# Optimization experiments

Measured on AMD Instinct MI355X. Metric: run time of the kernel, lower is better.

Reference implementation:

```python
import jax, jax.numpy as jnp
import numpy as np

FILTER_LENGTHS = (2, 4)  # from module: self.filter_length = [2, 4]


def _get_conv(signal, b, h, l, d_k, conv, w):
    # signal: [b, h*d_k, l] (raw reshape of [b,h,l,d_k], matching torch .reshape)
    f = max(FILTER_LENGTHS)
    pad = f // 2
    padded = jnp.pad(signal, ((0, 0), (0, 0), (pad, pad)))  # [b, d, l+f]
    # unfold(-1, f, 1)[:, :, :l, :] -> sliding windows, keep first l
    idx = jnp.arange(l)[:, None] + jnp.arange(f)[None, :]  # [l, f]
    seq = padded[:, :, idx]  # [b, d, l, f]
    # dynamic filter-length selection: w_f = filter_lengths * w, pick argmax
    f_s = jnp.asarray(FILTER_LENGTHS, dtype=signal.dtype)
    ind = jnp.argmax(f_s * w)
    chosen_len = jnp.asarray(FILTER_LENGTHS)[ind]
    mask = (jnp.arange(f) < chosen_len).astype(signal.dtype)  # [f]
    seq = seq * mask  # broadcast over [b, d, l, f]
    # depthwise-ish conv via einsum, then raw reshape (b, l, h*d_k) -> (b, h, l, d_k)
    out = jnp.einsum('bdlf,dof->blo', seq, conv)
    return out.reshape(b, h, l, d_k)


def reference(Q, K, V, attn_mask, conv_q, conv_k, w):
    b, h, l, d_k = Q.shape
    Qc = _get_conv(Q.reshape(b, h * d_k, l), b, h, l, d_k, conv_q, w) + Q
    Kc = _get_conv(K.reshape(b, h * d_k, l), b, h, l, d_k, conv_k, w) + K
    scores = jnp.einsum('bhqd,bhkd->bhqk', Qc, Kc) / np.sqrt(d_k).astype(Q.dtype)
    attn = jax.nn.softmax(scores, axis=-1)
    context = jnp.einsum('bhqk,bhkd->bhqd', attn, V)
    return context, attn


def setup_inputs() -> dict:
    key = jax.random.key(0)
    ks = jax.random.split(key, 6)
    b, h, l, d_k = 4, 8, 2048, 64
    d = h * d_k
    f = max(FILTER_LENGTHS)
    return {
        'Q': jax.random.normal(ks[0], (b, h, l, d_k), dtype=jnp.float32),
        'K': jax.random.normal(ks[1], (b, h, l, d_k), dtype=jnp.float32),
        'V': jax.random.normal(ks[2], (b, h, l, d_k), dtype=jnp.float32),
        'attn_mask': jnp.zeros((b, 1, l, l), dtype=bool),  # unused by forward
        'conv_q': jax.random.normal(ks[3], (d, d, f), dtype=jnp.float32),
        'conv_k': jax.random.normal(ks[4], (d, d, f), dtype=jnp.float32),
        'w': jax.random.normal(ks[5], (2,), dtype=jnp.float32),
    }
```

## Files before the change

### kernel.cpp

```cpp
#include <hip/hip_runtime.h>

typedef _Float16 f16;
typedef _Float16 f16x4 __attribute__((ext_vector_type(4)));
typedef _Float16 f16x8 __attribute__((ext_vector_type(8)));
typedef float f32x4 __attribute__((ext_vector_type(4)));
typedef float f32x16 __attribute__((ext_vector_type(16)));

#define MFMA32(A, B, C) __builtin_amdgcn_mfma_f32_32x32x16_f16(A, B, C, 0, 0, 0)

constexpr int Bb = 4, Hh = 8, Ll = 2048, Dk = 64, Dm = 512, BH = 32;

constexpr size_t NWF = (size_t)16 * 128 * 64 * 8;
constexpr size_t NFF = (size_t)BH * 64 * 4 * 64 * 8;
constexpr size_t NVF = (size_t)BH * 2 * 128 * 64 * 8;

constexpr size_t OFF_WF = 256;
constexpr size_t OFF_FF = OFF_WF + 4 * NWF * sizeof(f16);
constexpr size_t OFF_VF = OFF_FF + 4 * NFF * sizeof(f16);

#define QSCALE 0.1803368801111204f

__global__ void kprep_w(const float* __restrict__ convq, const float* __restrict__ convk,
                        const float* __restrict__ w, int* __restrict__ flag,
                        f16* __restrict__ wfhq, f16* __restrict__ wflq,
                        f16* __restrict__ wfhk, f16* __restrict__ wflk) {
    const int len = (4.f * w[1] > 2.f * w[0]) ? 4 : 2;
    if (blockIdx.x == 0 && blockIdx.y == 0 && threadIdx.x == 0) *flag = len;
    int g = blockIdx.x * 256 + threadIdx.x;
    int o = g & 511, c8 = g >> 9;
    const float* conv = blockIdx.y ? convk : convq;
    f16* dh = blockIdx.y ? wfhk : wfhq;
    f16* dl = blockIdx.y ? wflk : wflq;
    float4 v[8];
#pragma unroll
    for (int cc = 0; cc < 8; ++cc)
        v[cc] = *(const float4*)(conv + ((size_t)(c8 * 8 + cc) * 512 + o) * 4);
    int ob = o >> 5;
#pragma unroll
    for (int f = 0; f < 4; ++f) {
        f16x8 hv, lv;
#pragma unroll
        for (int cc = 0; cc < 8; ++cc) {
            float x = (f < len) ? ((const float*)&v[cc])[f] : 0.f;
            f16 hi = (f16)x;
            hv[cc] = hi; lv[cc] = (f16)(x - (float)hi);
        }
        int k16 = f * 32 + (c8 >> 1);
        size_t base = (((size_t)ob * 128 + k16) * 64 + (c8 & 1) * 32 + (o & 31)) * 8;
        *(f16x8*)(dh + base) = hv;
        *(f16x8*)(dl + base) = lv;
    }
}

__global__ void kprep_v(const float* __restrict__ V, f16* __restrict__ vf) {
    int bh = blockIdx.y, l0 = blockIdx.x * 128;
    int tid = threadIdx.x;
    const float* src = V + (size_t)bh * Ll * Dk;
#pragma unroll
    for (int s = 0; s < 4; ++s) {
        int g = s * 4 + (tid >> 6);
        int lane = tid & 63;
        int l16s = g >> 1, db = g & 1;
        int khalf = lane >> 5, lane31 = lane & 31;
        int d = db * 32 + lane31;
        f16x8 out;
#pragma unroll
        for (int j = 0; j < 8; ++j) {
            int l = l0 + l16s * 16 + khalf * 8 + j;
            out[j] = (f16)src[(size_t)l * Dk + d];
        }
        size_t idx = ((((size_t)bh * 2 + db) * 128 + (l0 >> 4) + l16s) * 64 + lane) * 8;
        *(f16x8*)(vf + idx) = out;
    }
}

__global__ __launch_bounds__(256, 4) void kconv(
    const float* __restrict__ Q, const float* __restrict__ K, const int* __restrict__ flag,
    const f16* __restrict__ wfhq, const f16* __restrict__ wflq,
    const f16* __restrict__ wfhk, const f16* __restrict__ wflk,
    f16* __restrict__ ffhq, f16* __restrict__ fflq,
    f16* __restrict__ ffhk, f16* __restrict__ fflk) {
    __shared__ __align__(16) f16 est[4][2][32][40];
    int id = blockIdx.x;
    int xcd = id & 7, oTile = (id >> 3) & 3, gidx = id >> 5;
    int g = gidx * 8 + xcd;
    int tt = g & 31, b = (g >> 5) & 3, tensor = (g >> 7) & 1;
    int wave = threadIdx.x >> 6, lane = threadIdx.x & 63;
    int wn = wave & 1, wm = wave >> 1;
    int lane31 = lane & 31, khalf = lane >> 5;
    const f16* bhp = (tensor ? wfhk : wfhq) + ((size_t)(oTile * 4 + wn * 2) * 128) * 512;
    const f16* blp = (tensor ? wflk : wflq) + ((size_t)(oTile * 4 + wn * 2) * 128) * 512;
    const float* src = (tensor ? K : Q) + (size_t)b * Dm * Ll;
    f16* dh = (tensor ? ffhk : ffhq);
    f16* dl = (tensor ? fflk : fflq);
    const float scale = tensor ? 1.f : QSCALE;
    const int klen16 = (*flag) << 5;
    const int t0 = (tt * 2 + wm) * 32;
    const int coff = khalf * 8;

    f32x16 acc[2];
#pragma unroll
    for (int j = 0; j < 2; ++j)
#pragma unroll
        for (int r = 0; r < 16; ++r) acc[j][r] = 0.f;

    f16x8 Abh[2], Abl[2], Bbh[2], Bbl[2];
    float XA[8], XB[8], mkA, mkB;
    const size_t lo8 = (size_t)lane * 8;

#define LOADX(X, MK, KN) do {                                                        \
    int f_ = (KN) >> 5;                                                              \
    int cb_ = (((KN) >> 2) & 7) * 64 + ((KN) & 3) * 16 + coff;                       \
    int t_ = t0 - 2 + lane31 + f_;                                                   \
    int tc_ = t_ < 0 ? 0 : (t_ > Ll - 1 ? Ll - 1 : t_);                              \
    MK = (t_ == tc_) ? 1.f : 0.f;                                                    \
    const float* sp_ = src + (size_t)cb_ * Ll + tc_;                                 \
    _Pragma("unroll") for (int j_ = 0; j_ < 8; ++j_) X[j_] = sp_[(size_t)j_ * Ll];   \
} while (0)

#define CVTA(X, MK, AH, AL) do {                                                     \
    _Pragma("unroll") for (int j_ = 0; j_ < 8; ++j_) {                               \
        float x_ = X[j_] * MK; f16 h_ = (f16)x_;                                     \
        AH[j_] = h_; AL[j_] = (f16)(x_ - (float)h_); }                               \
} while (0)

    LOADX(XA, mkA, 0);
    Abh[0] = *(const f16x8*)(bhp + lo8);
    Abl[0] = *(const f16x8*)(blp + lo8);
    Abh[1] = *(const f16x8*)(bhp + 128 * 512 + lo8);
    Abl[1] = *(const f16x8*)(blp + 128 * 512 + lo8);

    for (int k16 = 0; k16 < klen16; k16 += 2) {
        {
            int kn = k16 + 1;
            LOADX(XB, mkB, kn);
            size_t o = (size_t)kn * 512 + lo8;
            Bbh[0] = *(const f16x8*)(bhp + o);
            Bbl[0] = *(const f16x8*)(blp + o);
            Bbh[1] = *(const f16x8*)(bhp + 128 * 512 + o);
            Bbl[1] = *(const f16x8*)(blp + 128 * 512 + o);
        }
        {
            f16x8 Ah, Al;
            CVTA(XA, mkA, Ah, Al);
#pragma unroll
            for (int j = 0; j < 2; ++j) {
                acc[j] = MFMA32(Ah, Abh[j], acc[j]);
                acc[j] = MFMA32(Ah, Abl[j], acc[j]);
                acc[j] = MFMA32(Al, Abh[j], acc[j]);
            }
        }
        {
            int kn = k16 + 2 < klen16 ? k16 + 2 : klen16 - 1;
            LOADX(XA, mkA, kn);
            size_t o = (size_t)kn * 512 + lo8;
            Abh[0] = *(const f16x8*)(bhp + o);
            Abl[0] = *(const f16x8*)(blp + o);
            Abh[1] = *(const f16x8*)(bhp + 128 * 512 + o);
            Abl[1] = *(const f16x8*)(blp + 128 * 512 + o);
        }
        {
            f16x8 Bh, Bl;
            CVTA(XB, mkB, Bh, Bl);
#pragma unroll
            for (int j = 0; j < 2; ++j) {
                acc[j] = MFMA32(Bh, Bbh[j], acc[j]);
                acc[j] = MFMA32(Bh, Bbl[j], acc[j]);
                acc[j] = MFMA32(Bl, Bbh[j], acc[j]);
            }
        }
    }
#undef LOADX
#undef CVTA
    const int lcol = oTile * 2 + wn;
#pragma unroll
    for (int j = 0; j < 2; ++j) {
#pragma unroll
        for (int r = 0; r < 16; ++r) {
            int tl = (r & 3) + ((r >> 2) << 3) + (khalf << 2);
            int trow = tt * 64 + wm * 32 + tl;
            int h = trow >> 8;
            int l = ((trow & 255) << 3) + lcol;
            int d = j * 32 + lane31;
            float v2 = (acc[j][r] + src[((size_t)h * Ll + l) * Dk + d]) * scale;
            f16 hi = (f16)v2;
            est[wave][0][tl][lane31] = hi;
            est[wave][1][tl][lane31] = (f16)(v2 - (float)hi);
        }
        __asm__ volatile("s_waitcnt lgkmcnt(0)" ::: "memory");
#pragma unroll
        for (int c = 0; c < 2; ++c) {
            int id2 = c * 64 + lane;
            int row = id2 >> 2;
            int dc = id2 & 3;
            int trow = tt * 64 + wm * 32 + row;
            int h = trow >> 8;
            int l = ((trow & 255) << 3) + lcol;
            size_t base2 = ((size_t)(b * 8 + h) * 64 + (l >> 5)) * 4;
            size_t idx = (base2 + j * 2 + (dc >> 1)) * 512 + (size_t)(dc & 1) * 256 + (l & 31) * 8;
            f16x8 hv = *(const f16x8*)&est[wave][0][row][dc * 8];
            f16x8 lv = *(const f16x8*)&est[wave][1][row][dc * 8];
            *(f16x8*)(dh + idx) = hv;
            *(f16x8*)(dl + idx) = lv;
        }
        __asm__ volatile("s_waitcnt lgkmcnt(0)" ::: "memory");
    }
}

#define LOADK(DST, CH) do { size_t kb_ = (size_t)(CH) * 2048 + lane * 8;            \
    _Pragma("unroll") for (int ks_ = 0; ks_ < 4; ++ks_) {                           \
        DST[2 * ks_]     = *(const f16x8*)(kbh + kb_ + ks_ * 512);                  \
        DST[2 * ks_ + 1] = *(const f16x8*)(kbl + kb_ + ks_ * 512); } } while (0)

#define QKM(SRC, ACC) do { _Pragma("unroll") for (int ks_ = 0; ks_ < 4; ++ks_) {    \
        ACC = MFMA32(a_h[ks_], SRC[2 * ks_], ACC);                                  \
        ACC = MFMA32(a_h[ks_], SRC[2 * ks_ + 1], ACC);                              \
        ACC = MFMA32(a_l[ks_], SRC[2 * ks_], ACC); } } while (0)

#define SMUPD(ACC) do { _Pragma("unroll") for (int r_ = 0; r_ < 16; ++r_) {         \
        float v_ = ACC[r_]; float d_ = v_ - m[r_]; float e_ = exp2f(-fabsf(d_));    \
        bool gt_ = d_ > 0.f;                                                        \
        s[r_] = gt_ ? __fmaf_rn(s[r_], e_, 1.f) : (s[r_] + e_);                     \
        m[r_] = gt_ ? v_ : m[r_]; } } while (0)

#define LOADV(DST, CH) do { _Pragma("unroll") for (int q_ = 0; q_ < 4; ++q_) {      \
        int n_ = q_ >> 1, ks2_ = q_ & 1;                                            \
        size_t off_ = ((((size_t)bh * 2 + n_) * 128 + (CH) * 2 + ks2_) * 64 + lane) * 8; \
        DST[q_] = *(const f16x8*)(vf + off_); } } while (0)

union SMemU {
    float combuf[2][32][64];
    f16 sbuf[4][32][264];
};

__global__ __launch_bounds__(256, 2) void kattn(
    const f16* __restrict__ qfh, const f16* __restrict__ qfl,
    const f16* __restrict__ kfh, const f16* __restrict__ kfl,
    const f16* __restrict__ vf,
    float* __restrict__ ctx_out, float* __restrict__ attn_out) {
    __shared__ __align__(16) SMemU sm;
    int id = blockIdx.x;
    int bh = (id & 7) * 4 + (id >> 8);
    int qt = (id >> 3) & 31;
    int wave = threadIdx.x >> 6, lane = threadIdx.x & 63;
    int qg = wave >> 1, kg = wave & 1;
    int lane31 = lane & 31, khalf = lane >> 5;
    int q0 = qt * 64 + qg * 32;

    f16x8 a_h[4], a_l[4];
    {
        size_t qb = ((size_t)bh * 64 + qt * 2 + qg) * 4;
#pragma unroll
        for (int ks = 0; ks < 4; ++ks) {
            a_h[ks] = *(const f16x8*)(qfh + ((qb + ks) * 64 + lane) * 8);
            a_l[ks] = *(const f16x8*)(qfl + ((qb + ks) * 64 + lane) * 8);
        }
    }
    const f16* kbh = kfh + (size_t)bh * 131072;
    const f16* kbl = kfl + (size_t)bh * 131072;
    const int ch0 = kg * 32, ch1 = ch0 + 32;

    float m[16], s[16];
#pragma unroll
    for (int r = 0; r < 16; ++r) { m[r] = -3.0e38f; s[r] = 0.f; }

    {
        f16x8 KA[8], KB[8];
        LOADK(KA, ch0);
        for (int ch = ch0; ch < ch1; ch += 2) {
            LOADK(KB, ch + 1);
            f32x16 acc;
#pragma unroll
            for (int r = 0; r < 16; ++r) acc[r] = 0.f;
            QKM(KA, acc);
            SMUPD(acc);
            {
                int chn = (ch + 2 < ch1) ? ch + 2 : ch;
                LOADK(KA, chn);
            }
            f32x16 acc2;
#pragma unroll
            for (int r = 0; r < 16; ++r) acc2[r] = 0.f;
            QKM(KB, acc2);
            SMUPD(acc2);
        }
    }
#pragma unroll
    for (int r = 0; r < 16; ++r) {
        float mm = m[r], ss = s[r];
#pragma unroll
        for (int off = 1; off < 32; off <<= 1) {
            float mo = __shfl_xor(mm, off, 64);
            float so = __shfl_xor(ss, off, 64);
            float mn = fmaxf(mm, mo);
            ss = ss * exp2f(mm - mn) + so * exp2f(mo - mn);
            mm = mn;
        }
        m[r] = mm; s[r] = ss;
    }
    if (kg == 1) {
#pragma unroll
        for (int r = 0; r < 16; ++r) {
            sm.combuf[qg][r][lane] = m[r];
            sm.combuf[qg][16 + r][lane] = s[r];
        }
    }
    __syncthreads();
    if (kg == 0) {
#pragma unroll
        for (int r = 0; r < 16; ++r) {
            float m1 = sm.combuf[qg][r][lane];
            float s1 = sm.combuf[qg][16 + r][lane];
            float mn = fmaxf(m[r], m1);
            float ss = s[r] * exp2f(m[r] - mn) + s1 * exp2f(m1 - mn);
            m[r] = mn; s[r] = 1.f / ss;
            sm.combuf[qg][r][lane] = mn;
            sm.combuf[qg][16 + r][lane] = s[r];
        }
    }
    __syncthreads();
    if (kg == 1) {
#pragma unroll
        for (int r = 0; r < 16; ++r) {
            m[r] = sm.combuf[qg][r][lane];
            s[r] = sm.combuf[qg][16 + r][lane];
        }
    }
    __syncthreads();

    f32x16 ctx[2];
#pragma unroll
    for (int n = 0; n < 2; ++n)
#pragma unroll
        for (int r = 0; r < 16; ++r) ctx[n][r] = 0.f;

    const size_t rowbase = ((size_t)bh * Ll + q0) * Ll;

    {
        f16x8 KV[8], VV[4];
        LOADK(KV, ch0);
        LOADV(VV, ch0);
        for (int chb = ch0; chb < ch1; chb += 8) {
#pragma unroll
            for (int i = 0; i < 8; ++i) {
                int ch = chb + i;
                f32x16 acc;
#pragma unroll
                for (int r = 0; r < 16; ++r) acc[r] = 0.f;
                QKM(KV, acc);
                int chn = (ch + 1 < ch1) ? ch + 1 : ch;
                LOADK(KV, chn);
#pragma unroll
                for (int r = 0; r < 16; ++r) {
                    float p = exp2f(acc[r] - m[r]) * s[r];
                    int row = (r & 3) + ((r >> 2) << 3) + (khalf << 2);
                    sm.sbuf[wave][row][i * 32 + lane31] = (f16)p;
                }
                __asm__ volatile("s_waitcnt lgkmcnt(0)" ::: "memory");
#pragma unroll
                for (int ks2 = 0; ks2 < 2; ++ks2) {
                    f16x8 pa = *(const f16x8*)&sm.sbuf[wave][lane31][i * 32 + ks2 * 16 + khalf * 8];
                    ctx[0] = MFMA32(pa, VV[ks2], ctx[0]);
                    ctx[1] = MFMA32(pa, VV[2 + ks2], ctx[1]);
                }
                LOADV(VV, chn);
            }
#pragma unroll
            for (int ri = 0; ri < 16; ++ri) {
                int row = ri * 2 + khalf;
                f16x8 pv = *(const f16x8*)&sm.sbuf[wave][row][lane31 * 8];
                f32x4 o0 = {(float)pv[0], (float)pv[1], (float)pv[2], (float)pv[3]};
                f32x4 o1 = {(float)pv[4], (float)pv[5], (float)pv[6], (float)pv[7]};
                float* dst = attn_out + rowbase + (size_t)row * Ll + chb * 32 + lane31 * 8;
                *(f32x4*)dst = o0;
                *(f32x4*)(dst + 4) = o1;
            }
        }
    }
    __syncthreads();
    if (kg == 1) {
#pragma unroll
        for (int n = 0; n < 2; ++n)
#pragma unroll
            for (int r = 0; r < 16; ++r) sm.combuf[qg][n * 16 + r][lane] = ctx[n][r];
    }
    __syncthreads();
    if (kg == 0) {
#pragma unroll
        for (int n = 0; n < 2; ++n)
#pragma unroll
            for (int r = 0; r < 16; ++r) {
                float v = ctx[n][r] + sm.combuf[qg][n * 16 + r][lane];
                int row = (r & 3) + ((r >> 2) << 3) + (khalf << 2);
                ctx_out[((size_t)bh * Ll + q0 + row) * Dk + n * 32 + lane31] = v;
            }
    }
}

extern "C" void kernel_launch(void* const* d_in, const int* in_sizes, int n_in,
                              void* d_out, int out_size, void* d_ws, size_t ws_size,
                              hipStream_t stream) {
    const float* Q = (const float*)d_in[0];
    const float* K = (const float*)d_in[1];
    const float* V = (const float*)d_in[2];
    const float* convq = (const float*)d_in[4];
    const float* convk = (const float*)d_in[5];
    const float* w = (const float*)d_in[6];

    char* ws = (char*)d_ws;
    int* flag = (int*)ws;
    f16* wfhq = (f16*)(ws + OFF_WF);
    f16* wflq = wfhq + NWF;
    f16* wfhk = wflq + NWF;
    f16* wflk = wfhk + NWF;
    f16* ffhq = (f16*)(ws + OFF_FF);
    f16* fflq = ffhq + NFF;
    f16* ffhk = fflq + NFF;
    f16* fflk = ffhk + NFF;
    f16* vf = (f16*)(ws + OFF_VF);

    float* ctx_out = (float*)d_out;
    float* attn_out = ctx_out + (size_t)BH * Ll * Dk;

    kprep_w<<<dim3(128, 2), 256, 0, stream>>>(convq, convk, w, flag, wfhq, wflq, wfhk, wflk);
    kprep_v<<<dim3(16, 32), 256, 0, stream>>>(V, vf);
    kconv<<<dim3(1024), 256, 0, stream>>>(Q, K, flag,
                                          wfhq, wflq, wfhk, wflk, ffhq, fflq, ffhk, fflk);
    kattn<<<dim3(1024), 256, 0, stream>>>(ffhq, fflq, ffhk, fflk, vf, ctx_out, attn_out);
}
```

Baseline: 965.7 us.

## Double-buffer attention probability staging and interleave attn stores with compute

Splits the per-wave shared-memory staging buffer into two halves of four key chunks each and alternates between them. The global write of the previous group's attention probabilities is spread across the MFMA iterations of the current group rather than done as one burst after every eight chunks. The aim is to overlap the large attention-matrix write traffic with compute. In exchange the stores become narrower per lane (four floats instead of eight), and the epilogue has to flush the last buffer separately.

```diff
diff --git a/kernel.cpp b/kernel.cpp
--- a/kernel.cpp
+++ b/kernel.cpp
@@ -230,7 +230,7 @@
 
 union SMemU {
     float combuf[2][32][64];
-    f16 sbuf[4][32][264];
+    f16 sbuf[2][4][32][136];
 };
 
 __global__ __launch_bounds__(256, 2) void kattn(
@@ -340,9 +340,10 @@
         f16x8 KV[8], VV[4];
         LOADK(KV, ch0);
         LOADV(VV, ch0);
-        for (int chb = ch0; chb < ch1; chb += 8) {
-#pragma unroll
-            for (int i = 0; i < 8; ++i) {
+        int sst = 0;
+        for (int chb = ch0; chb < ch1; chb += 4, sst ^= 1) {
+#pragma unroll
+            for (int i = 0; i < 4; ++i) {
                 int ch = chb + i;
                 f32x16 acc;
 #pragma unroll
@@ -354,26 +355,37 @@
                 for (int r = 0; r < 16; ++r) {
                     float p = exp2f(acc[r] - m[r]) * s[r];
                     int row = (r & 3) + ((r >> 2) << 3) + (khalf << 2);
-                    sm.sbuf[wave][row][i * 32 + lane31] = (f16)p;
+                    sm.sbuf[sst][wave][row][i * 32 + lane31] = (f16)p;
                 }
                 __asm__ volatile("s_waitcnt lgkmcnt(0)" ::: "memory");
 #pragma unroll
                 for (int ks2 = 0; ks2 < 2; ++ks2) {
-                    f16x8 pa = *(const f16x8*)&sm.sbuf[wave][lane31][i * 32 + ks2 * 16 + khalf * 8];
+                    f16x8 pa = *(const f16x8*)&sm.sbuf[sst][wave][lane31][i * 32 + ks2 * 16 + khalf * 8];
                     ctx[0] = MFMA32(pa, VV[ks2], ctx[0]);
                     ctx[1] = MFMA32(pa, VV[2 + ks2], ctx[1]);
                 }
                 LOADV(VV, chn);
-            }
+                if (chb > ch0) {
+                    int chbp = chb - 4;
+#pragma unroll
+                    for (int q = 0; q < 4; ++q) {
+                        int ri = i * 4 + q;
+                        int row = ri * 2 + khalf;
+                        f16x4 pv = *(const f16x4*)&sm.sbuf[sst ^ 1][wave][row][lane31 * 4];
+                        f32x4 o = {(float)pv[0], (float)pv[1], (float)pv[2], (float)pv[3]};
+                        *(f32x4*)(attn_out + rowbase + (size_t)row * Ll + chbp * 32 + lane31 * 4) = o;
+                    }
+                }
+            }
+        }
+        {
+            int chbp = ch1 - 4;
 #pragma unroll
             for (int ri = 0; ri < 16; ++ri) {
                 int row = ri * 2 + khalf;
-                f16x8 pv = *(const f16x8*)&sm.sbuf[wave][row][lane31 * 8];
-                f32x4 o0 = {(float)pv[0], (float)pv[1], (float)pv[2], (float)pv[3]};
-                f32x4 o1 = {(float)pv[4], (float)pv[5], (float)pv[6], (float)pv[7]};
-                float* dst = attn_out + rowbase + (size_t)row * Ll + chb * 32 + lane31 * 8;
-                *(f32x4*)dst = o0;
-                *(f32x4*)(dst + 4) = o1;
+                f16x4 pv = *(const f16x4*)&sm.sbuf[sst ^ 1][wave][row][lane31 * 4];
+                f32x4 o = {(float)pv[0], (float)pv[1], (float)pv[2], (float)pv[3]};
+                *(f32x4*)(attn_out + rowbase + (size_t)row * Ll + chbp * 32 + lane31 * 4) = o;
             }
         }
     }
```

New measurement: 915.2 us. -5.2%, faster.
